# Kernel optimization log

Hardware: AMD Instinct MI355X
Metric: run time of the kernel (lower is better)

The kernel has to match this reference:

```python
import jax, jax.numpy as jnp
import numpy as np

E = 100000          # number of edges
IN_FEATS = 256      # in_edge_feats
HIDDEN = 128        # hidden_size
K = 16              # neighbors per edge (uniform-degree rendering of ragged lists)


def setup_inputs() -> dict:
    key = jax.random.key(0)
    k1, k2, k3, k4 = jax.random.split(key, 4)
    edge_feats = jax.random.normal(k1, (E, IN_FEATS), dtype=jnp.float32)
    neighbors = jax.random.randint(k2, (E, K), 0, E, dtype=jnp.int32)
    # Linear params (torch Linear: y = x @ W^T + b; here W stored as [in, out])
    W = jax.random.normal(k3, (IN_FEATS, HIDDEN), dtype=jnp.float32) / np.sqrt(IN_FEATS)
    b = jax.random.normal(k4, (HIDDEN,), dtype=jnp.float32) * 0.01
    return {"edge_feats": edge_feats, "neighbors": neighbors, "W": W, "b": b}


def reference(edge_feats, neighbors, W, b):
    # Dense linear transform of all edge features: [E, H]
    t = edge_feats @ W + b
    # Gather each edge's K neighbor transformed features and sum: [E, K, H] -> [E, H]
    nbr_sum = jnp.take(t, neighbors, axis=0).sum(axis=1)
    # agg[i] = t[i] + sum_{n in neighbors[i]} t[n]
    return t + nbr_sum
```

## Files before the change

### kernel.cpp

```cpp
#include <hip/hip_runtime.h>
#include <hip/hip_bf16.h>
#include <stdint.h>

#define E_EDGES 100000
#define IN_F    256
#define HID     128
#define KNB     16

typedef short bf16x8 __attribute__((ext_vector_type(8)));
typedef float f32x4  __attribute__((ext_vector_type(4)));

__device__ __forceinline__ unsigned short f2bf(float f) {
    union { float f; unsigned u; } v; v.f = f;
    unsigned u = v.u;
    u += 0x7fffu + ((u >> 16) & 1u);
    return (unsigned short)(u >> 16);
}

__global__ void conv_w_kernel(const float* __restrict__ W, unsigned short* __restrict__ Wt) {
    int t = blockIdx.x * blockDim.x + threadIdx.x;
    int n = t & (HID - 1);
    int k = t >> 7;
    Wt[(size_t)n * IN_F + k] = f2bf(W[(size_t)k * HID + n]);
}

__launch_bounds__(256)
__global__ void gemm_t_kernel(const float* __restrict__ A,
                              const unsigned short* __restrict__ Wt,
                              const float* __restrict__ bias,
                              unsigned short* __restrict__ T) {
    __shared__ unsigned short Bs[32768];
    const int tid  = threadIdx.x;
    const int wave = tid >> 6;
    const int lane = tid & 63;
    const int l15  = lane & 15;
    const int quad = lane >> 4;
    const int rowbase = blockIdx.x * 64 + wave * 16;
    int arow = rowbase + l15;
    if (arow >= E_EDGES) arow = E_EDGES - 1;

    const float* ap = A + (size_t)arow * IN_F + quad * 8;
    float4 af32[16];
    #pragma unroll
    for (int k0 = 0; k0 < 8; ++k0) {
        af32[2 * k0]     = *(const float4*)(ap + k0 * 32);
        af32[2 * k0 + 1] = *(const float4*)(ap + k0 * 32 + 4);
    }

    #pragma unroll
    for (int it = 0; it < 16; ++it) {
        int e    = it * 256 + tid;
        int n    = e >> 5;
        int k8   = e & 31;
        int dst  = ((k8 >> 2) * 8 + (n >> 4)) * 64 + (k8 & 3) * 16 + (n & 15);
        uint4 v = *(const uint4*)(Wt + (size_t)e * 8);
        *(uint4*)(Bs + (size_t)dst * 8) = v;
    }
    __syncthreads();

    bf16x8 apre[8];
    #pragma unroll
    for (int k0 = 0; k0 < 8; ++k0) {
        float4 lo = af32[2 * k0], hi = af32[2 * k0 + 1];
        bf16x8 f;
        f[0] = (short)f2bf(lo.x); f[1] = (short)f2bf(lo.y);
        f[2] = (short)f2bf(lo.z); f[3] = (short)f2bf(lo.w);
        f[4] = (short)f2bf(hi.x); f[5] = (short)f2bf(hi.y);
        f[6] = (short)f2bf(hi.z); f[7] = (short)f2bf(hi.w);
        apre[k0] = f;
    }

    f32x4 acc[8] = {};
    #pragma unroll
    for (int k0 = 0; k0 < 8; ++k0) {
        #pragma unroll
        for (int ct = 0; ct < 8; ++ct) {
            bf16x8 bf = *(const bf16x8*)(Bs + ((size_t)((k0 * 8 + ct) * 64 + lane)) * 8);
            acc[ct] = __builtin_amdgcn_mfma_f32_16x16x32_bf16(apre[k0], bf, acc[ct], 0, 0, 0);
        }
    }

    #pragma unroll
    for (int ct = 0; ct < 8; ++ct) {
        const int col = ct * 16 + l15;
        const float bv = bias[col];
        #pragma unroll
        for (int i = 0; i < 4; ++i) {
            const int row = rowbase + quad * 4 + i;
            if (row < E_EDGES)
                T[(size_t)row * HID + col] = f2bf(acc[ct][i] + bv);
        }
    }
}

__launch_bounds__(256)
__global__ void gather_sum_kernel(const unsigned short* __restrict__ T,
                                  const int* __restrict__ nbr,
                                  float* __restrict__ out) {
    __shared__ int sidx[256];
    const int tid   = threadIdx.x;
    const int edge0 = blockIdx.x * 16;
    sidx[tid] = nbr[(size_t)edge0 * KNB + tid];
    __syncthreads();

    const int el   = tid >> 4;
    const int lane = tid & 15;
    const int edge = edge0 + el;

    float acc[8];
    {
        uint4 v = *(const uint4*)(T + (size_t)edge * HID + lane * 8);
        unsigned w[4] = { v.x, v.y, v.z, v.w };
        union { unsigned u; float f; } c;
        #pragma unroll
        for (int j = 0; j < 4; ++j) {
            c.u = w[j] << 16;          acc[2 * j]     = c.f;
            c.u = w[j] & 0xffff0000u;  acc[2 * j + 1] = c.f;
        }
    }
    #pragma unroll
    for (int k = 0; k < KNB; ++k) {
        const int n = sidx[el * KNB + k];
        uint4 v = *(const uint4*)(T + (size_t)n * HID + lane * 8);
        unsigned w[4] = { v.x, v.y, v.z, v.w };
        union { unsigned u; float f; } c;
        #pragma unroll
        for (int j = 0; j < 4; ++j) {
            c.u = w[j] << 16;          acc[2 * j]     += c.f;
            c.u = w[j] & 0xffff0000u;  acc[2 * j + 1] += c.f;
        }
    }

    float* op = out + (size_t)edge * HID + lane * 8;
    f32x4 o0 = { acc[0], acc[1], acc[2], acc[3] };
    f32x4 o1 = { acc[4], acc[5], acc[6], acc[7] };
    __builtin_nontemporal_store(o0, (f32x4*)op);
    __builtin_nontemporal_store(o1, (f32x4*)(op + 4));
}

extern "C" void kernel_launch(void* const* d_in, const int* in_sizes, int n_in,
                              void* d_out, int out_size, void* d_ws, size_t ws_size,
                              hipStream_t stream) {
    const float* edge_feats = (const float*)d_in[0];
    const int*   neighbors  = (const int*)d_in[1];
    const float* W          = (const float*)d_in[2];
    const float* b          = (const float*)d_in[3];
    float*       out        = (float*)d_out;

    unsigned short* Wt = (unsigned short*)d_ws;
    unsigned short* T  = (unsigned short*)d_ws + (size_t)IN_F * HID;

    conv_w_kernel<<<(IN_F * HID) / 256, 256, 0, stream>>>(W, Wt);
    gemm_t_kernel<<<(E_EDGES + 63) / 64, 256, 0, stream>>>(edge_feats, Wt, b, T);
    gather_sum_kernel<<<E_EDGES / 16, 256, 0, stream>>>(T, neighbors, out);
}
```

Baseline: 245.7 us.

## Persistent GEMM with preswizzled weights and batched gather loads

The weight conversion kernel now writes bf16 weights directly in the MFMA fragment layout, so the GEMM copies them into shared memory linearly. The GEMM becomes a persistent grid of 512 blocks that loops over row chunks, loading the weights and bias once per block instead of once per 64 rows. The gather kernel issues all 17 row loads before any accumulation, separated by a scheduling barrier, to raise memory-level parallelism. Output stores change from nontemporal to plain stores. The costs are higher register pressure in the gather, and less latency hiding in the GEMM because each block processes its chunks one after another.

Measured after the change: 263.4 us. +7.2%, slower.

```diff
diff --git a/kernel.cpp b/kernel.cpp
--- a/kernel.cpp
+++ b/kernel.cpp
@@ -6,6 +6,8 @@
 #define IN_F    256
 #define HID     128
 #define KNB     16
+#define NCHUNK  ((E_EDGES + 63) / 64)
+#define GEMM_GRID 512
 
 typedef short bf16x8 __attribute__((ext_vector_type(8)));
 typedef float f32x4  __attribute__((ext_vector_type(4)));
@@ -17,16 +19,27 @@
     return (unsigned short)(u >> 16);
 }
 
-__global__ void conv_w_kernel(const float* __restrict__ W, unsigned short* __restrict__ Wt) {
-    int t = blockIdx.x * blockDim.x + threadIdx.x;
-    int n = t & (HID - 1);
-    int k = t >> 7;
-    Wt[(size_t)n * IN_F + k] = f2bf(W[(size_t)k * HID + n]);
+__global__ void conv_w_kernel(const float* __restrict__ W, unsigned short* __restrict__ Wtf) {
+    int d = blockIdx.x * 256 + threadIdx.x;
+    int f = d >> 6, L = d & 63;
+    int k0 = f >> 3, ct = f & 7, quad = L >> 4, l15 = L & 15;
+    int n  = ct * 16 + l15;
+    int kb = (k0 * 4 + quad) * 8;
+    const float* wp = W + (size_t)kb * HID + n;
+    unsigned short h[8];
+    #pragma unroll
+    for (int j = 0; j < 8; ++j) h[j] = f2bf(wp[(size_t)j * HID]);
+    uint4 o;
+    o.x = (unsigned)h[0] | ((unsigned)h[1] << 16);
+    o.y = (unsigned)h[2] | ((unsigned)h[3] << 16);
+    o.z = (unsigned)h[4] | ((unsigned)h[5] << 16);
+    o.w = (unsigned)h[6] | ((unsigned)h[7] << 16);
+    *(uint4*)(Wtf + (size_t)d * 8) = o;
 }
 
-__launch_bounds__(256)
+__launch_bounds__(256, 2)
 __global__ void gemm_t_kernel(const float* __restrict__ A,
-                              const unsigned short* __restrict__ Wt,
+                              const unsigned short* __restrict__ Wtf,
                               const float* __restrict__ bias,
                               unsigned short* __restrict__ T) {
     __shared__ unsigned short Bs[32768];
@@ -35,60 +48,63 @@
     const int lane = tid & 63;
     const int l15  = lane & 15;
     const int quad = lane >> 4;
-    const int rowbase = blockIdx.x * 64 + wave * 16;
-    int arow = rowbase + l15;
-    if (arow >= E_EDGES) arow = E_EDGES - 1;
-
-    const float* ap = A + (size_t)arow * IN_F + quad * 8;
-    float4 af32[16];
-    #pragma unroll
-    for (int k0 = 0; k0 < 8; ++k0) {
-        af32[2 * k0]     = *(const float4*)(ap + k0 * 32);
-        af32[2 * k0 + 1] = *(const float4*)(ap + k0 * 32 + 4);
-    }
 
     #pragma unroll
     for (int it = 0; it < 16; ++it) {
-        int e    = it * 256 + tid;
-        int n    = e >> 5;
-        int k8   = e & 31;
-        int dst  = ((k8 >> 2) * 8 + (n >> 4)) * 64 + (k8 & 3) * 16 + (n & 15);
-        uint4 v = *(const uint4*)(Wt + (size_t)e * 8);
-        *(uint4*)(Bs + (size_t)dst * 8) = v;
+        int d = it * 256 + tid;
+        *(uint4*)(Bs + (size_t)d * 8) = *(const uint4*)(Wtf + (size_t)d * 8);
     }
+
+    float bv[8];
+    #pragma unroll
+    for (int ct = 0; ct < 8; ++ct) bv[ct] = bias[ct * 16 + l15];
+
     __syncthreads();
 
-    bf16x8 apre[8];
-    #pragma unroll
-    for (int k0 = 0; k0 < 8; ++k0) {
-        float4 lo = af32[2 * k0], hi = af32[2 * k0 + 1];
-        bf16x8 f;
-        f[0] = (short)f2bf(lo.x); f[1] = (short)f2bf(lo.y);
-        f[2] = (short)f2bf(lo.z); f[3] = (short)f2bf(lo.w);
-        f[4] = (short)f2bf(hi.x); f[5] = (short)f2bf(hi.y);
-        f[6] = (short)f2bf(hi.z); f[7] = (short)f2bf(hi.w);
-        apre[k0] = f;
-    }
+    for (int c = blockIdx.x; c < NCHUNK; c += GEMM_GRID) {
+        const int rowbase = c * 64 + wave * 16;
+        int arow = rowbase + l15;
+        if (arow >= E_EDGES) arow = E_EDGES - 1;
 
-    f32x4 acc[8] = {};
-    #pragma unroll
-    for (int k0 = 0; k0 < 8; ++k0) {
+        const float* ap = A + (size_t)arow * IN_F + quad * 8;
+        float4 af32[16];
+        #pragma unroll
+        for (int k0 = 0; k0 < 8; ++k0) {
+            af32[2 * k0]     = *(const float4*)(ap + k0 * 32);
+            af32[2 * k0 + 1] = *(const float4*)(ap + k0 * 32 + 4);
+        }
+
+        bf16x8 apre[8];
+        #pragma unroll
+        for (int k0 = 0; k0 < 8; ++k0) {
+            float4 lo = af32[2 * k0], hi = af32[2 * k0 + 1];
+            bf16x8 f;
+            f[0] = (short)f2bf(lo.x); f[1] = (short)f2bf(lo.y);
+            f[2] = (short)f2bf(lo.z); f[3] = (short)f2bf(lo.w);
+            f[4] = (short)f2bf(hi.x); f[5] = (short)f2bf(hi.y);
+            f[6] = (short)f2bf(hi.z); f[7] = (short)f2bf(hi.w);
+            apre[k0] = f;
+        }
+
+        f32x4 acc[8] = {};
+        #pragma unroll
+        for (int k0 = 0; k0 < 8; ++k0) {
+            #pragma unroll
+            for (int ct = 0; ct < 8; ++ct) {
+                bf16x8 bf = *(const bf16x8*)(Bs + ((size_t)((k0 * 8 + ct) * 64 + lane)) * 8);
+                acc[ct] = __builtin_amdgcn_mfma_f32_16x16x32_bf16(apre[k0], bf, acc[ct], 0, 0, 0);
+            }
+        }
+
         #pragma unroll
         for (int ct = 0; ct < 8; ++ct) {
-            bf16x8 bf = *(const bf16x8*)(Bs + ((size_t)((k0 * 8 + ct) * 64 + lane)) * 8);
-            acc[ct] = __builtin_amdgcn_mfma_f32_16x16x32_bf16(apre[k0], bf, acc[ct], 0, 0, 0);
-        }
-    }
-
-    #pragma unroll
-    for (int ct = 0; ct < 8; ++ct) {
-        const int col = ct * 16 + l15;
-        const float bv = bias[col];
-        #pragma unroll
-        for (int i = 0; i < 4; ++i) {
-            const int row = rowbase + quad * 4 + i;
-            if (row < E_EDGES)
-                T[(size_t)row * HID + col] = f2bf(acc[ct][i] + bv);
+            const int col = ct * 16 + l15;
+            #pragma unroll
+            for (int i = 0; i < 4; ++i) {
+                const int row = rowbase + quad * 4 + i;
+                if (row < E_EDGES)
+                    T[(size_t)row * HID + col] = f2bf(acc[ct][i] + bv[ct]);
+            }
         }
     }
 }
@@ -107,22 +123,18 @@
     const int lane = tid & 15;
     const int edge = edge0 + el;
 
-    float acc[8];
-    {
-        uint4 v = *(const uint4*)(T + (size_t)edge * HID + lane * 8);
-        unsigned w[4] = { v.x, v.y, v.z, v.w };
-        union { unsigned u; float f; } c;
-        #pragma unroll
-        for (int j = 0; j < 4; ++j) {
-            c.u = w[j] << 16;          acc[2 * j]     = c.f;
-            c.u = w[j] & 0xffff0000u;  acc[2 * j + 1] = c.f;
-        }
-    }
+    const unsigned short* tb = T + (size_t)lane * 8;
+    uint4 v[17];
+    v[0] = *(const uint4*)(tb + (size_t)edge * HID);
     #pragma unroll
-    for (int k = 0; k < KNB; ++k) {
-        const int n = sidx[el * KNB + k];
-        uint4 v = *(const uint4*)(T + (size_t)n * HID + lane * 8);
-        unsigned w[4] = { v.x, v.y, v.z, v.w };
+    for (int k = 0; k < KNB; ++k)
+        v[k + 1] = *(const uint4*)(tb + (size_t)sidx[el * KNB + k] * HID);
+    __builtin_amdgcn_sched_barrier(0);
+
+    float acc[8] = {};
+    #pragma unroll
+    for (int k = 0; k < 17; ++k) {
+        unsigned w[4] = { v[k].x, v[k].y, v[k].z, v[k].w };
         union { unsigned u; float f; } c;
         #pragma unroll
         for (int j = 0; j < 4; ++j) {
@@ -132,10 +144,10 @@
     }
 
     float* op = out + (size_t)edge * HID + lane * 8;
-    f32x4 o0 = { acc[0], acc[1], acc[2], acc[3] };
-    f32x4 o1 = { acc[4], acc[5], acc[6], acc[7] };
-    __builtin_nontemporal_store(o0, (f32x4*)op);
-    __builtin_nontemporal_store(o1, (f32x4*)(op + 4));
+    float4 o0 = { acc[0], acc[1], acc[2], acc[3] };
+    float4 o1 = { acc[4], acc[5], acc[6], acc[7] };
+    *(float4*)op       = o0;
+    *(float4*)(op + 4) = o1;
 }
 
 extern "C" void kernel_launch(void* const* d_in, const int* in_sizes, int n_in,
@@ -147,10 +159,10 @@
     const float* b          = (const float*)d_in[3];
     float*       out        = (float*)d_out;
 
-    unsigned short* Wt = (unsigned short*)d_ws;
-    unsigned short* T  = (unsigned short*)d_ws + (size_t)IN_F * HID;
+    unsigned short* Wtf = (unsigned short*)d_ws;
+    unsigned short* T   = (unsigned short*)d_ws + (size_t)IN_F * HID;
 
-    conv_w_kernel<<<(IN_F * HID) / 256, 256, 0, stream>>>(W, Wt);
-    gemm_t_kernel<<<(E_EDGES + 63) / 64, 256, 0, stream>>>(edge_feats, Wt, b, T);
+    conv_w_kernel<<<16, 256, 0, stream>>>(W, Wtf);
+    gemm_t_kernel<<<GEMM_GRID, 256, 0, stream>>>(edge_feats, Wtf, b, T);
     gather_sum_kernel<<<E_EDGES / 16, 256, 0, stream>>>(T, neighbors, out);
 }
```
